# Kernel tuning notes

Hardware: AMD Instinct MI355X
Metric: run time of the kernel (lower is better)

Reference implementation:

```python
import jax, jax.numpy as jnp
import numpy as np

NUM_NODE = 5000
EMBED_DIM = 256
NUM_CLS = 20
EDGE_ROWS = (NUM_NODE - 1) * (NUM_NODE - 1) + 1  # 24990002
BZ, SEQ, NBR = 64, 512, 16


def setup_inputs() -> dict:
    key = jax.random.key(0)
    k = jax.random.split(key, 8)
    X = jax.random.randint(k[0], (BZ, SEQ), 0, NUM_NODE)
    NX = jax.random.randint(k[1], (BZ, SEQ, NBR), 0, NUM_NODE)
    EW = jax.random.randint(k[2], (BZ, SEQ, NBR), 0, EDGE_ROWS)
    # parameters (xavier-ish scale); padding_idx=0 rows zeroed
    node_emb = jax.random.normal(k[3], (NUM_NODE, EMBED_DIM), jnp.float32) * 0.02
    node_emb = node_emb.at[0].set(0.0)
    edge_w = jax.random.normal(k[4], (EDGE_ROWS, 1), jnp.float32) * 0.02
    edge_w = edge_w.at[0].set(0.0)
    node_w = jax.random.normal(k[5], (NUM_NODE, 1), jnp.float32) * 0.02
    node_w = node_w.at[0].set(0.0)
    fc_W = jax.random.normal(k[6], (NUM_CLS, EMBED_DIM), jnp.float32) * 0.05
    fc_b = jnp.zeros((NUM_CLS,), jnp.float32)
    return {"X": X, "NX": NX, "EW": EW, "node_emb": node_emb,
            "edge_w": edge_w, "node_w": node_w, "fc_W": fc_W, "fc_b": fc_b}


def reference(X, NX, EW, node_emb, edge_w, node_w, fc_W, fc_b):
    Ra = node_emb[NX]                      # (bz, seq, nbr, d) neighbor embeddings
    Ean = edge_w[EW]                       # (bz, seq, nbr, 1) edge weights
    Mn = jnp.max(Ra * Ean, axis=2)         # (bz, seq, d) max over neighbors
    Rn = node_emb[X]                       # (bz, seq, d)
    Nn = node_w[X]                         # (bz, seq, 1)
    y = (1.0 - Nn) * Mn + Nn * Rn          # weighted combine
    y = jnp.sum(y, axis=1)                 # (bz, d) sum-pool over sequence
    y = y @ fc_W.T + fc_b                  # (bz, num_cls)
    y = jax.nn.relu(y)
    # Dropout is identity at inference; LogSoftmax over dim=1
    return jax.nn.log_softmax(y, axis=1)
```

## Files before the change

kernel.cpp:

```cpp
#include <hip/hip_runtime.h>
#include <math.h>

#define NUM_NODE 5000
#define BZ   64
#define SEQ  512
#define NBR  16
#define DIM  256
#define NCLS 20

#define ROWB  (DIM * 2)
#define NCHUNK2 (SEQ / 4)
#define NCHUNK16 (SEQ / 16)

__device__ __forceinline__ int bcast_i(int v, int lane) {
    return __builtin_amdgcn_readlane(v, lane);
}
__device__ __forceinline__ float bcast_f(float v, int lane) {
    return __int_as_float(__builtin_amdgcn_readlane(__float_as_int(v), lane));
}
__device__ __forceinline__ unsigned bf16_rne(float f) {
    unsigned u = __float_as_uint(f);
    return (u + 0x7fffu + ((u >> 16) & 1u)) >> 16;
}
__device__ __forceinline__ float lo_bf16(unsigned u) { return __uint_as_float(u << 16); }
__device__ __forceinline__ float hi_bf16(unsigned u) { return __uint_as_float(u & 0xffff0000u); }

__global__ __launch_bounds__(256) void zero_ws_kernel(float* __restrict__ ws, int n) {
    int i = blockIdx.x * blockDim.x + threadIdx.x;
    if (i < n) ws[i] = 0.0f;
}

__global__ __launch_bounds__(256) void cvt_emb_zero_kernel(
    const float4* __restrict__ src, uint2* __restrict__ dst, int n4,
    float* __restrict__ ypre, int nacc) {
    int i = blockIdx.x * blockDim.x + threadIdx.x;
    if (i < n4) {
        float4 v = src[i];
        uint2 o;
        o.x = bf16_rne(v.x) | (bf16_rne(v.y) << 16);
        o.y = bf16_rne(v.z) | (bf16_rne(v.w) << 16);
        dst[i] = o;
    }
    if (i < nacc) ypre[i] = 0.0f;
}

__global__ __launch_bounds__(256, 8) void gnn_gather_kernel(
    const int*   __restrict__ X,
    const int*   __restrict__ NX,
    const int*   __restrict__ EW,
    const char*  __restrict__ embb,
    const float* __restrict__ edge_w,
    const float* __restrict__ node_w,
    float*       __restrict__ ypre)
{
    __shared__ float lds[4][DIM];

    const int b     = blockIdx.x / NCHUNK2;
    const int chunk = blockIdx.x % NCHUNK2;
    const int wave  = threadIdx.x >> 6;
    const int lane  = threadIdx.x & 63;
    const int half  = lane >> 5;
    const int sub   = lane & 31;
    const int voff  = sub * 16;

    const int s  = chunk * 4 + wave;
    const int bs = b * SEQ + s;

    int   nxv = 0;
    float ewv = 0.f;
    if (lane < NBR) {
        nxv = __builtin_nontemporal_load(&NX[bs * NBR + lane]);
        const int ewi = __builtin_nontemporal_load(&EW[bs * NBR + lane]);
        ewv = __builtin_nontemporal_load(&edge_w[ewi]);
    }
    const int   x  = X[bs];
    const float nn = node_w[x];

    uint4 e[8];
    #pragma unroll
    for (int j = 0; j < 8; ++j) {
        const int n0 = bcast_i(nxv, 2 * j);
        const int n1 = bcast_i(nxv, 2 * j + 1);
        const int n  = half ? n1 : n0;
        e[j] = *(const uint4*)(embb + (size_t)n * ROWB + voff);
    }
    const uint4 es = *(const uint4*)(embb + (size_t)x * ROWB + voff);

    float m[8];
    #pragma unroll
    for (int i = 0; i < 8; ++i) m[i] = -INFINITY;

    #pragma unroll
    for (int j = 0; j < 8; ++j) {
        const float w0 = bcast_f(ewv, 2 * j);
        const float w1 = bcast_f(ewv, 2 * j + 1);
        const float w  = half ? w1 : w0;
        m[0] = fmaxf(m[0], lo_bf16(e[j].x) * w);
        m[1] = fmaxf(m[1], hi_bf16(e[j].x) * w);
        m[2] = fmaxf(m[2], lo_bf16(e[j].y) * w);
        m[3] = fmaxf(m[3], hi_bf16(e[j].y) * w);
        m[4] = fmaxf(m[4], lo_bf16(e[j].z) * w);
        m[5] = fmaxf(m[5], hi_bf16(e[j].z) * w);
        m[6] = fmaxf(m[6], lo_bf16(e[j].w) * w);
        m[7] = fmaxf(m[7], hi_bf16(e[j].w) * w);
    }

    #pragma unroll
    for (int i = 0; i < 8; ++i)
        m[i] = fmaxf(m[i], __shfl_xor(m[i], 32));

    const float om = 1.0f - nn;
    float acc[8];
    acc[0] = om * m[0] + nn * lo_bf16(es.x);
    acc[1] = om * m[1] + nn * hi_bf16(es.x);
    acc[2] = om * m[2] + nn * lo_bf16(es.y);
    acc[3] = om * m[3] + nn * hi_bf16(es.y);
    acc[4] = om * m[4] + nn * lo_bf16(es.z);
    acc[5] = om * m[5] + nn * hi_bf16(es.z);
    acc[6] = om * m[6] + nn * lo_bf16(es.w);
    acc[7] = om * m[7] + nn * hi_bf16(es.w);

    if (half == 0) {
        *(float4*)&lds[wave][8 * sub]     = make_float4(acc[0], acc[1], acc[2], acc[3]);
        *(float4*)&lds[wave][8 * sub + 4] = make_float4(acc[4], acc[5], acc[6], acc[7]);
    }
    __syncthreads();

    const int t = threadIdx.x;
    atomicAdd(&ypre[b * DIM + t], lds[0][t] + lds[1][t] + lds[2][t] + lds[3][t]);
}

__global__ __launch_bounds__(256) void gnn_gather_f32_kernel(
    const int*   __restrict__ X,
    const int*   __restrict__ NX,
    const int*   __restrict__ EW,
    const float* __restrict__ node_emb,
    const float* __restrict__ edge_w,
    const float* __restrict__ node_w,
    float*       __restrict__ dst)
{
    __shared__ float lds[4][DIM];
    const int b     = blockIdx.x / NCHUNK16;
    const int chunk = blockIdx.x % NCHUNK16;
    const int wave  = threadIdx.x >> 6;
    const int lane  = threadIdx.x & 63;
    const int s0  = chunk * 16 + wave * 4;
    const int bs0 = b * SEQ + s0;

    const int   nx  = NX[bs0 * NBR + lane];
    const float ew  = edge_w[EW[bs0 * NBR + lane]];
    int xv = 0; float nwv = 0.f;
    if (lane < 4) { xv = X[bs0 + lane]; nwv = node_w[xv]; }

    float4 acc = make_float4(0.f, 0.f, 0.f, 0.f);
    for (int p = 0; p < 4; ++p) {
        float4 m = make_float4(-INFINITY, -INFINITY, -INFINITY, -INFINITY);
        for (int k = 0; k < NBR; ++k) {
            const int   n = bcast_i(nx, p * 16 + k);
            const float w = bcast_f(ew, p * 16 + k);
            const float4 e = *(const float4*)(node_emb + (size_t)n * DIM + 4 * lane);
            m.x = fmaxf(m.x, e.x * w); m.y = fmaxf(m.y, e.y * w);
            m.z = fmaxf(m.z, e.z * w); m.w = fmaxf(m.w, e.w * w);
        }
        const int   x  = bcast_i(xv, p);
        const float nn = bcast_f(nwv, p);
        const float om = 1.0f - nn;
        const float4 r = *(const float4*)(node_emb + (size_t)x * DIM + 4 * lane);
        acc.x += om * m.x + nn * r.x; acc.y += om * m.y + nn * r.y;
        acc.z += om * m.z + nn * r.z; acc.w += om * m.w + nn * r.w;
    }
    *(float4*)&lds[wave][4 * lane] = acc;
    __syncthreads();
    const int t = threadIdx.x;
    atomicAdd(&dst[b * DIM + t], lds[0][t] + lds[1][t] + lds[2][t] + lds[3][t]);
}

__global__ __launch_bounds__(256) void gnn_head_kernel(
    const float* __restrict__ ypre,
    const float* __restrict__ fc_W,
    const float* __restrict__ fc_b,
    float*       __restrict__ out)
{
    __shared__ float vals[NCLS];
    __shared__ float lse;

    const int b = blockIdx.x;
    const int t = threadIdx.x;
    const int wave = t >> 6;
    const int lane = t & 63;

    const float4 y4 = *(const float4*)(ypre + b * DIM + 4 * lane);

    #pragma unroll
    for (int ci = 0; ci < 5; ++ci) {
        const int c = wave * 5 + ci;
        const float4 w4 = *(const float4*)(fc_W + c * DIM + 4 * lane);
        float d = y4.x * w4.x + y4.y * w4.y + y4.z * w4.z + y4.w * w4.w;
        #pragma unroll
        for (int off = 32; off; off >>= 1) d += __shfl_xor(d, off);
        if (lane == 0) vals[c] = fmaxf(d + fc_b[c], 0.0f);
    }
    __syncthreads();

    if (t == 0) {
        float mx = -INFINITY;
        for (int c = 0; c < NCLS; ++c) mx = fmaxf(mx, vals[c]);
        float s = 0.0f;
        for (int c = 0; c < NCLS; ++c) s += expf(vals[c] - mx);
        lse = mx + logf(s);
    }
    __syncthreads();

    if (t < NCLS) out[b * NCLS + t] = vals[t] - lse;
}

extern "C" void kernel_launch(void* const* d_in, const int* in_sizes, int n_in,
                              void* d_out, int out_size, void* d_ws, size_t ws_size,
                              hipStream_t stream) {
    const int*   X        = (const int*)  d_in[0];
    const int*   NX       = (const int*)  d_in[1];
    const int*   EW       = (const int*)  d_in[2];
    const float* node_emb = (const float*)d_in[3];
    const float* edge_w   = (const float*)d_in[4];
    const float* node_w   = (const float*)d_in[5];
    const float* fc_W     = (const float*)d_in[6];
    const float* fc_b     = (const float*)d_in[7];
    float* out = (float*)d_out;

    const size_t acc_bytes = (size_t)BZ * DIM * sizeof(float);
    const size_t emb_bytes = (size_t)NUM_NODE * DIM * sizeof(unsigned short);
    float* ypre = (float*)d_ws;
    char*  embb = (char*)d_ws + acc_bytes;

    if (ws_size >= acc_bytes + emb_bytes) {
        const int n4 = NUM_NODE * DIM / 4;
        cvt_emb_zero_kernel<<<(n4 + 255) / 256, 256, 0, stream>>>(
            (const float4*)node_emb, (uint2*)embb, n4, ypre, BZ * DIM);
        gnn_gather_kernel<<<BZ * NCHUNK2, 256, 0, stream>>>(
            X, NX, EW, embb, edge_w, node_w, ypre);
        gnn_head_kernel<<<BZ, 256, 0, stream>>>(ypre, fc_W, fc_b, out);
    } else {
        zero_ws_kernel<<<(BZ * DIM + 255) / 256, 256, 0, stream>>>(ypre, BZ * DIM);
        gnn_gather_f32_kernel<<<BZ * NCHUNK16, 256, 0, stream>>>(
            X, NX, EW, node_emb, edge_w, node_w, ypre);
        gnn_head_kernel<<<BZ, 256, 0, stream>>>(ypre, fc_W, fc_b, out);
    }
}
```

Measured before the change: 176.8 us.

## Pre-gather edge weights in the prep kernel to decouple random loads from gather

```diff
diff --git a/kernel.cpp b/kernel.cpp
--- a/kernel.cpp
+++ b/kernel.cpp
@@ -12,6 +12,11 @@
 #define NCHUNK2 (SEQ / 4)
 #define NCHUNK16 (SEQ / 16)
 
+#define N4        (NUM_NODE * DIM / 4)
+#define CVT_BLOCKS ((N4 + 255) / 256)
+#define EWP_N     (BZ * SEQ * NBR)
+#define EWP_BLOCKS (EWP_N / 256)
+
 __device__ __forceinline__ int bcast_i(int v, int lane) {
     return __builtin_amdgcn_readlane(v, lane);
 }
@@ -30,26 +35,37 @@
     if (i < n) ws[i] = 0.0f;
 }
 
-__global__ __launch_bounds__(256) void cvt_emb_zero_kernel(
-    const float4* __restrict__ src, uint2* __restrict__ dst, int n4,
-    float* __restrict__ ypre, int nacc) {
-    int i = blockIdx.x * blockDim.x + threadIdx.x;
-    if (i < n4) {
-        float4 v = src[i];
-        uint2 o;
-        o.x = bf16_rne(v.x) | (bf16_rne(v.y) << 16);
-        o.y = bf16_rne(v.z) | (bf16_rne(v.w) << 16);
-        dst[i] = o;
-    }
-    if (i < nacc) ypre[i] = 0.0f;
+__global__ __launch_bounds__(256) void prep_kernel(
+    const float4* __restrict__ src,
+    uint2*        __restrict__ dst,
+    float*        __restrict__ ypre,
+    const int*    __restrict__ EW,
+    const float*  __restrict__ edge_w,
+    float*        __restrict__ ews)
+{
+    const int bid = blockIdx.x;
+    if (bid < CVT_BLOCKS) {
+        int i = bid * 256 + threadIdx.x;
+        if (i < N4) {
+            float4 v = src[i];
+            uint2 o;
+            o.x = bf16_rne(v.x) | (bf16_rne(v.y) << 16);
+            o.y = bf16_rne(v.z) | (bf16_rne(v.w) << 16);
+            dst[i] = o;
+        }
+        if (i < BZ * DIM) ypre[i] = 0.0f;
+    } else {
+        int i = (bid - CVT_BLOCKS) * 256 + threadIdx.x;
+        const int ewi = __builtin_nontemporal_load(&EW[i]);
+        ews[i] = __builtin_nontemporal_load(&edge_w[ewi]);
+    }
 }
 
 __global__ __launch_bounds__(256, 8) void gnn_gather_kernel(
     const int*   __restrict__ X,
     const int*   __restrict__ NX,
-    const int*   __restrict__ EW,
+    const float* __restrict__ ews,
     const char*  __restrict__ embb,
-    const float* __restrict__ edge_w,
     const float* __restrict__ node_w,
     float*       __restrict__ ypre)
 {
@@ -70,8 +86,7 @@
     float ewv = 0.f;
     if (lane < NBR) {
         nxv = __builtin_nontemporal_load(&NX[bs * NBR + lane]);
-        const int ewi = __builtin_nontemporal_load(&EW[bs * NBR + lane]);
-        ewv = __builtin_nontemporal_load(&edge_w[ewi]);
+        ewv = ews[bs * NBR + lane];
     }
     const int   x  = X[bs];
     const float nn = node_w[x];
@@ -229,15 +244,16 @@
 
     const size_t acc_bytes = (size_t)BZ * DIM * sizeof(float);
     const size_t emb_bytes = (size_t)NUM_NODE * DIM * sizeof(unsigned short);
+    const size_t ews_bytes = (size_t)EWP_N * sizeof(float);
     float* ypre = (float*)d_ws;
     char*  embb = (char*)d_ws + acc_bytes;
-
-    if (ws_size >= acc_bytes + emb_bytes) {
-        const int n4 = NUM_NODE * DIM / 4;
-        cvt_emb_zero_kernel<<<(n4 + 255) / 256, 256, 0, stream>>>(
-            (const float4*)node_emb, (uint2*)embb, n4, ypre, BZ * DIM);
+    float* ews  = (float*)((char*)d_ws + acc_bytes + emb_bytes);
+
+    if (ws_size >= acc_bytes + emb_bytes + ews_bytes) {
+        prep_kernel<<<CVT_BLOCKS + EWP_BLOCKS, 256, 0, stream>>>(
+            (const float4*)node_emb, (uint2*)embb, ypre, EW, edge_w, ews);
         gnn_gather_kernel<<<BZ * NCHUNK2, 256, 0, stream>>>(
-            X, NX, EW, embb, edge_w, node_w, ypre);
+            X, NX, ews, embb, node_w, ypre);
         gnn_head_kernel<<<BZ, 256, 0, stream>>>(ypre, fc_W, fc_b, out);
     } else {
         zero_ws_kernel<<<(BZ * DIM + 255) / 256, 256, 0, stream>>>(ypre, BZ * DIM);
```

Result: slower. 183.5 us (+3.8%).

## Store gathered node embeddings as scaled FP8 instead of BF16

Applied to the files above, without the earlier changes.

```diff
diff --git a/kernel.cpp b/kernel.cpp
--- a/kernel.cpp
+++ b/kernel.cpp
@@ -8,22 +8,29 @@
 #define DIM  256
 #define NCLS 20
 
-#define ROWB  (DIM * 2)
+#define ROWB8 DIM
 #define NCHUNK2 (SEQ / 4)
 #define NCHUNK16 (SEQ / 16)
+#define N4 (NUM_NODE * DIM / 4)
+#define EMB_SCALE 256.0f
+#define INV_SCALE (1.0f / 256.0f)
+
+typedef float floatx2 __attribute__((ext_vector_type(2)));
 
 __device__ __forceinline__ int bcast_i(int v, int lane) {
     return __builtin_amdgcn_readlane(v, lane);
 }
-__device__ __forceinline__ float bcast_f(float v, int lane) {
-    return __int_as_float(__builtin_amdgcn_readlane(__float_as_int(v), lane));
-}
-__device__ __forceinline__ unsigned bf16_rne(float f) {
-    unsigned u = __float_as_uint(f);
-    return (u + 0x7fffu + ((u >> 16) & 1u)) >> 16;
-}
-__device__ __forceinline__ float lo_bf16(unsigned u) { return __uint_as_float(u << 16); }
-__device__ __forceinline__ float hi_bf16(unsigned u) { return __uint_as_float(u & 0xffff0000u); }
+__device__ __forceinline__ unsigned pack4_fp8(float4 v) {
+    int r = __builtin_amdgcn_cvt_pk_fp8_f32(v.x, v.y, 0, false);
+    r = __builtin_amdgcn_cvt_pk_fp8_f32(v.z, v.w, r, true);
+    return (unsigned)r;
+}
+__device__ __forceinline__ floatx2 unpk_lo(unsigned u) {
+    return __builtin_amdgcn_cvt_pk_f32_fp8((int)u, false);
+}
+__device__ __forceinline__ floatx2 unpk_hi(unsigned u) {
+    return __builtin_amdgcn_cvt_pk_f32_fp8((int)u, true);
+}
 
 __global__ __launch_bounds__(256) void zero_ws_kernel(float* __restrict__ ws, int n) {
     int i = blockIdx.x * blockDim.x + threadIdx.x;
@@ -31,27 +38,25 @@
 }
 
 __global__ __launch_bounds__(256) void cvt_emb_zero_kernel(
-    const float4* __restrict__ src, uint2* __restrict__ dst, int n4,
+    const float4* __restrict__ src, unsigned* __restrict__ dst, int n4,
     float* __restrict__ ypre, int nacc) {
     int i = blockIdx.x * blockDim.x + threadIdx.x;
     if (i < n4) {
         float4 v = src[i];
-        uint2 o;
-        o.x = bf16_rne(v.x) | (bf16_rne(v.y) << 16);
-        o.y = bf16_rne(v.z) | (bf16_rne(v.w) << 16);
-        dst[i] = o;
+        v.x *= EMB_SCALE; v.y *= EMB_SCALE; v.z *= EMB_SCALE; v.w *= EMB_SCALE;
+        dst[i] = pack4_fp8(v);
     }
     if (i < nacc) ypre[i] = 0.0f;
 }
 
-__global__ __launch_bounds__(256, 8) void gnn_gather_kernel(
-    const int*   __restrict__ X,
-    const int*   __restrict__ NX,
-    const int*   __restrict__ EW,
-    const char*  __restrict__ embb,
-    const float* __restrict__ edge_w,
-    const float* __restrict__ node_w,
-    float*       __restrict__ ypre)
+__global__ __launch_bounds__(256, 6) void gnn_gather_kernel(
+    const int*           __restrict__ X,
+    const int*           __restrict__ NX,
+    const int*           __restrict__ EW,
+    const unsigned char* __restrict__ emb8,
+    const float*         __restrict__ edge_w,
+    const float*         __restrict__ node_w,
+    float*               __restrict__ ypre)
 {
     __shared__ float lds[4][DIM];
 
@@ -59,9 +64,8 @@
     const int chunk = blockIdx.x % NCHUNK2;
     const int wave  = threadIdx.x >> 6;
     const int lane  = threadIdx.x & 63;
-    const int half  = lane >> 5;
-    const int sub   = lane & 31;
-    const int voff  = sub * 16;
+    const int q     = lane >> 4;
+    const int u     = lane & 15;
 
     const int s  = chunk * 4 + wave;
     const int bs = b * SEQ + s;
@@ -71,58 +75,60 @@
     if (lane < NBR) {
         nxv = __builtin_nontemporal_load(&NX[bs * NBR + lane]);
         const int ewi = __builtin_nontemporal_load(&EW[bs * NBR + lane]);
-        ewv = __builtin_nontemporal_load(&edge_w[ewi]);
+        ewv = __builtin_nontemporal_load(&edge_w[ewi]) * INV_SCALE;
     }
     const int   x  = X[bs];
     const float nn = node_w[x];
 
-    uint4 e[8];
-    #pragma unroll
-    for (int j = 0; j < 8; ++j) {
-        const int n0 = bcast_i(nxv, 2 * j);
-        const int n1 = bcast_i(nxv, 2 * j + 1);
-        const int n  = half ? n1 : n0;
-        e[j] = *(const uint4*)(embb + (size_t)n * ROWB + voff);
-    }
-    const uint4 es = *(const uint4*)(embb + (size_t)x * ROWB + voff);
-
-    float m[8];
-    #pragma unroll
-    for (int i = 0; i < 8; ++i) m[i] = -INFINITY;
-
-    #pragma unroll
-    for (int j = 0; j < 8; ++j) {
-        const float w0 = bcast_f(ewv, 2 * j);
-        const float w1 = bcast_f(ewv, 2 * j + 1);
-        const float w  = half ? w1 : w0;
-        m[0] = fmaxf(m[0], lo_bf16(e[j].x) * w);
-        m[1] = fmaxf(m[1], hi_bf16(e[j].x) * w);
-        m[2] = fmaxf(m[2], lo_bf16(e[j].y) * w);
-        m[3] = fmaxf(m[3], hi_bf16(e[j].y) * w);
-        m[4] = fmaxf(m[4], lo_bf16(e[j].z) * w);
-        m[5] = fmaxf(m[5], hi_bf16(e[j].z) * w);
-        m[6] = fmaxf(m[6], lo_bf16(e[j].w) * w);
-        m[7] = fmaxf(m[7], hi_bf16(e[j].w) * w);
-    }
-
-    #pragma unroll
-    for (int i = 0; i < 8; ++i)
-        m[i] = fmaxf(m[i], __shfl_xor(m[i], 32));
-
-    const float om = 1.0f - nn;
-    float acc[8];
-    acc[0] = om * m[0] + nn * lo_bf16(es.x);
-    acc[1] = om * m[1] + nn * hi_bf16(es.x);
-    acc[2] = om * m[2] + nn * lo_bf16(es.y);
-    acc[3] = om * m[3] + nn * hi_bf16(es.y);
-    acc[4] = om * m[4] + nn * lo_bf16(es.z);
-    acc[5] = om * m[5] + nn * hi_bf16(es.z);
-    acc[6] = om * m[6] + nn * lo_bf16(es.w);
-    acc[7] = om * m[7] + nn * hi_bf16(es.w);
-
-    if (half == 0) {
-        *(float4*)&lds[wave][8 * sub]     = make_float4(acc[0], acc[1], acc[2], acc[3]);
-        *(float4*)&lds[wave][8 * sub + 4] = make_float4(acc[4], acc[5], acc[6], acc[7]);
+    uint4 e[4];
+    #pragma unroll
+    for (int j = 0; j < 4; ++j) {
+        const int n = __shfl(nxv, j * 4 + q);
+        e[j] = *(const uint4*)(emb8 + (size_t)n * ROWB8 + u * 16);
+    }
+    const uint4 es = *(const uint4*)(emb8 + (size_t)x * ROWB8 + u * 16);
+
+    float m[16];
+    #pragma unroll
+    for (int i = 0; i < 16; ++i) m[i] = -INFINITY;
+
+    #pragma unroll
+    for (int j = 0; j < 4; ++j) {
+        const float w = __shfl(ewv, j * 4 + q);
+        floatx2 p;
+        p = unpk_lo(e[j].x); m[0]  = fmaxf(m[0],  p.x * w); m[1]  = fmaxf(m[1],  p.y * w);
+        p = unpk_hi(e[j].x); m[2]  = fmaxf(m[2],  p.x * w); m[3]  = fmaxf(m[3],  p.y * w);
+        p = unpk_lo(e[j].y); m[4]  = fmaxf(m[4],  p.x * w); m[5]  = fmaxf(m[5],  p.y * w);
+        p = unpk_hi(e[j].y); m[6]  = fmaxf(m[6],  p.x * w); m[7]  = fmaxf(m[7],  p.y * w);
+        p = unpk_lo(e[j].z); m[8]  = fmaxf(m[8],  p.x * w); m[9]  = fmaxf(m[9],  p.y * w);
+        p = unpk_hi(e[j].z); m[10] = fmaxf(m[10], p.x * w); m[11] = fmaxf(m[11], p.y * w);
+        p = unpk_lo(e[j].w); m[12] = fmaxf(m[12], p.x * w); m[13] = fmaxf(m[13], p.y * w);
+        p = unpk_hi(e[j].w); m[14] = fmaxf(m[14], p.x * w); m[15] = fmaxf(m[15], p.y * w);
+    }
+
+    #pragma unroll
+    for (int i = 0; i < 16; ++i) m[i] = fmaxf(m[i], __shfl_xor(m[i], 16));
+    #pragma unroll
+    for (int i = 0; i < 16; ++i) m[i] = fmaxf(m[i], __shfl_xor(m[i], 32));
+
+    const float om  = 1.0f - nn;
+    const float nns = nn * INV_SCALE;
+
+    if (q == 0) {
+        float acc[16];
+        floatx2 p;
+        p = unpk_lo(es.x); acc[0]  = om * m[0]  + nns * p.x; acc[1]  = om * m[1]  + nns * p.y;
+        p = unpk_hi(es.x); acc[2]  = om * m[2]  + nns * p.x; acc[3]  = om * m[3]  + nns * p.y;
+        p = unpk_lo(es.y); acc[4]  = om * m[4]  + nns * p.x; acc[5]  = om * m[5]  + nns * p.y;
+        p = unpk_hi(es.y); acc[6]  = om * m[6]  + nns * p.x; acc[7]  = om * m[7]  + nns * p.y;
+        p = unpk_lo(es.z); acc[8]  = om * m[8]  + nns * p.x; acc[9]  = om * m[9]  + nns * p.y;
+        p = unpk_hi(es.z); acc[10] = om * m[10] + nns * p.x; acc[11] = om * m[11] + nns * p.y;
+        p = unpk_lo(es.w); acc[12] = om * m[12] + nns * p.x; acc[13] = om * m[13] + nns * p.y;
+        p = unpk_hi(es.w); acc[14] = om * m[14] + nns * p.x; acc[15] = om * m[15] + nns * p.y;
+        #pragma unroll
+        for (int c = 0; c < 4; ++c)
+            *(float4*)&lds[wave][16 * u + 4 * c] =
+                make_float4(acc[4*c], acc[4*c+1], acc[4*c+2], acc[4*c+3]);
     }
     __syncthreads();
 
@@ -157,13 +163,13 @@
         float4 m = make_float4(-INFINITY, -INFINITY, -INFINITY, -INFINITY);
         for (int k = 0; k < NBR; ++k) {
             const int   n = bcast_i(nx, p * 16 + k);
-            const float w = bcast_f(ew, p * 16 + k);
+            const float w = __int_as_float(__builtin_amdgcn_readlane(__float_as_int(ew), p * 16 + k));
             const float4 e = *(const float4*)(node_emb + (size_t)n * DIM + 4 * lane);
             m.x = fmaxf(m.x, e.x * w); m.y = fmaxf(m.y, e.y * w);
             m.z = fmaxf(m.z, e.z * w); m.w = fmaxf(m.w, e.w * w);
         }
         const int   x  = bcast_i(xv, p);
-        const float nn = bcast_f(nwv, p);
+        const float nn = __int_as_float(__builtin_amdgcn_readlane(__float_as_int(nwv), p));
         const float om = 1.0f - nn;
         const float4 r = *(const float4*)(node_emb + (size_t)x * DIM + 4 * lane);
         acc.x += om * m.x + nn * r.x; acc.y += om * m.y + nn * r.y;
@@ -228,16 +234,15 @@
     float* out = (float*)d_out;
 
     const size_t acc_bytes = (size_t)BZ * DIM * sizeof(float);
-    const size_t emb_bytes = (size_t)NUM_NODE * DIM * sizeof(unsigned short);
-    float* ypre = (float*)d_ws;
-    char*  embb = (char*)d_ws + acc_bytes;
+    const size_t emb_bytes = (size_t)NUM_NODE * DIM;
+    float*         ypre = (float*)d_ws;
+    unsigned char* emb8 = (unsigned char*)d_ws + acc_bytes;
 
     if (ws_size >= acc_bytes + emb_bytes) {
-        const int n4 = NUM_NODE * DIM / 4;
-        cvt_emb_zero_kernel<<<(n4 + 255) / 256, 256, 0, stream>>>(
-            (const float4*)node_emb, (uint2*)embb, n4, ypre, BZ * DIM);
+        cvt_emb_zero_kernel<<<(N4 + 255) / 256, 256, 0, stream>>>(
+            (const float4*)node_emb, (unsigned*)emb8, N4, ypre, BZ * DIM);
         gnn_gather_kernel<<<BZ * NCHUNK2, 256, 0, stream>>>(
-            X, NX, EW, embb, edge_w, node_w, ypre);
+            X, NX, EW, emb8, edge_w, node_w, ypre);
         gnn_head_kernel<<<BZ, 256, 0, stream>>>(ypre, fc_W, fc_b, out);
     } else {
         zero_ws_kernel<<<(BZ * DIM + 255) / 256, 256, 0, stream>>>(ypre, BZ * DIM);
```

Result: no change. 176.9 us (+0.1%).
